# Kernel tuning notes

Measured on AMD Instinct MI355X. Metric: run time of the kernel, lower is better.

Reference implementation:

```python
import jax, jax.numpy as jnp
import numpy as np

N_NODES = 100000
N_EDGES = 1600000
IN_DIM, HID_DIM, OUT_DIM = 128, 64, 64


def setup_inputs() -> dict:
    key = jax.random.key(0)
    ks = jax.random.split(key, 7)
    x = jax.random.normal(ks[0], (N_NODES, IN_DIM), dtype=jnp.float32)
    edge_index = jax.random.randint(ks[1], (2, N_EDGES), 0, N_NODES, dtype=jnp.int64)
    user_idx = jax.random.randint(ks[2], (N_NODES,), 0, N_NODES, dtype=jnp.int64)
    W1 = jax.random.normal(ks[3], (IN_DIM, HID_DIM), dtype=jnp.float32) * (1.0 / np.sqrt(IN_DIM))
    b1 = jax.random.normal(ks[4], (HID_DIM,), dtype=jnp.float32) * 0.02
    W2 = jax.random.normal(ks[5], (HID_DIM, OUT_DIM), dtype=jnp.float32) * (1.0 / np.sqrt(HID_DIM))
    b2 = jax.random.normal(ks[6], (OUT_DIM,), dtype=jnp.float32) * 0.02
    return {"x": x, "edge_index": edge_index, "user_idx": user_idx,
            "W1": W1, "b1": b1, "W2": W2, "b2": b2}


def _gcn_conv(x, edge_index, W, b):
    # PyG GCNConv: linear transform, add self-loops, sym-normalized aggregation.
    N = x.shape[0]
    h = x @ W  # [N, F_out]
    loop = jnp.arange(N, dtype=edge_index.dtype)
    src = jnp.concatenate([edge_index[0], loop])  # [E+N]
    dst = jnp.concatenate([edge_index[1], loop])
    deg = jax.ops.segment_sum(jnp.ones(src.shape[0], dtype=h.dtype), dst, num_segments=N)
    dis = jnp.where(deg > 0, jax.lax.rsqrt(jnp.maximum(deg, 1.0)), 0.0)  # deg^{-1/2}
    norm = dis[src] * dis[dst]  # [E+N]
    msg = h[src] * norm[:, None]  # gather + scale
    out = jax.ops.segment_sum(msg, dst, num_segments=N)  # scatter-add at targets
    return out + b


def _scatter_mean(x, idx, dim_size):
    s = jax.ops.segment_sum(x, idx, num_segments=dim_size)
    cnt = jax.ops.segment_sum(jnp.ones(x.shape[0], dtype=x.dtype), idx, num_segments=dim_size)
    return jnp.where(cnt[:, None] > 0, s / jnp.maximum(cnt[:, None], 1.0), 0.0)


def reference(x, edge_index, user_idx, W1, b1, W2, b2):
    h = _gcn_conv(x, edge_index, W1, b1)
    h = jax.nn.relu(h)
    # dropout is identity in eval mode
    h = _gcn_conv(h, edge_index, W2, b2)
    return _scatter_mean(h, user_idx, h.shape[0])
```

## Files before the change

kernel.cpp:

```cpp
#include <hip/hip_runtime.h>
#include <hip/hip_bf16.h>


#define FEAT 64
#define INDIM 128

#define SCAN_BS 256
#define SCAN_ELEMS 8
#define SCAN_CHUNK (SCAN_BS * SCAN_ELEMS)

#define BIN_SHIFT 9
#define BIN_R 512
#define BIN_TILE 4096
#define BH_TILE 8192

typedef __attribute__((ext_vector_type(8))) short short8;
typedef __attribute__((ext_vector_type(4))) float f32x4;

__device__ __forceinline__ unsigned short f2bf(float f) {
    unsigned u = __float_as_uint(f);
    unsigned r = u + 0x7FFFu + ((u >> 16) & 1u);
    return (unsigned short)(r >> 16);
}
__device__ __forceinline__ float bf2f(unsigned short v) {
    return __uint_as_float(((unsigned)v) << 16);
}


__global__ __launch_bounds__(256) void k_bhist(const int* __restrict__ dst,
                                               int* __restrict__ gbc, int E, int N, int KB) {
    __shared__ int h[256];
    const int tid = threadIdx.x;
    h[tid] = 0;
    __syncthreads();
    const int base = blockIdx.x * BH_TILE;
    #pragma unroll
    for (int t = 0; t < BH_TILE / 256; ++t) {
        int e = base + t * 256 + tid;
        if (e < E) {
            int d = dst[e];
            if ((unsigned)d < (unsigned)N) atomicAdd(&h[d >> BIN_SHIFT], 1);
        }
    }
    __syncthreads();
    if (tid < KB && h[tid]) atomicAdd(&gbc[tid], h[tid]);
}

__global__ __launch_bounds__(256) void k_bscan(const int* __restrict__ gbc,
                                               int* __restrict__ bb,
                                               int* __restrict__ bcur,
                                               int* __restrict__ rpN, int KB) {
    __shared__ int lds[256];
    const int tid = threadIdx.x;
    int v = (tid < KB) ? gbc[tid] : 0;
    lds[tid] = v;
    __syncthreads();
    for (int d = 1; d < 256; d <<= 1) {
        int t = (tid >= d) ? lds[tid - d] : 0;
        __syncthreads();
        lds[tid] += t;
        __syncthreads();
    }
    int excl = lds[tid] - v;
    if (tid < KB) { bb[tid] = excl; bcur[tid] = excl; }
    if (tid == 255) { bb[KB] = lds[255]; *rpN = lds[255]; }
}

__global__ __launch_bounds__(256) void k_binA(const int* __restrict__ src,
                                              const int* __restrict__ dst,
                                              int* __restrict__ bcur,
                                              unsigned* __restrict__ pairs,
                                              int E, int N, int KB) {
    __shared__ unsigned lbuf[BIN_TILE];
    __shared__ unsigned short bkt[BIN_TILE];
    __shared__ int lcnt[256];
    __shared__ int loff[256];
    __shared__ int lbase[256];
    __shared__ int tot;
    const int tid = threadIdx.x;
    const int base = blockIdx.x * BIN_TILE;

    lcnt[tid] = 0;
    __syncthreads();

    int mys[16], myd[16], myb[16];
    #pragma unroll
    for (int t = 0; t < 16; ++t) {
        int e = base + t * 256 + tid;
        int s = 0, d = -1;
        if (e < E) { s = src[e]; d = dst[e]; }
        if ((unsigned)d >= (unsigned)N) d = -1;
        if ((unsigned)s >= (unsigned)N) s = 0;
        mys[t] = s; myd[t] = d;
        myb[t] = (d >= 0) ? (d >> BIN_SHIFT) : -1;
        if (myb[t] >= 0) atomicAdd(&lcnt[myb[t]], 1);
    }
    __syncthreads();

    int v = lcnt[tid];
    loff[tid] = v;
    __syncthreads();
    for (int d = 1; d < 256; d <<= 1) {
        int t2 = (tid >= d) ? loff[tid - d] : 0;
        __syncthreads();
        loff[tid] += t2;
        __syncthreads();
    }
    if (tid == 255) tot = loff[255];
    int excl = loff[tid] - v;
    __syncthreads();
    loff[tid] = excl;
    lcnt[tid] = excl;
    if (tid < KB && v > 0) lbase[tid] = atomicAdd(&bcur[tid], v);
    __syncthreads();

    #pragma unroll
    for (int t = 0; t < 16; ++t) {
        if (myb[t] >= 0) {
            int pos = atomicAdd(&lcnt[myb[t]], 1);
            lbuf[pos] = ((unsigned)mys[t] << BIN_SHIFT) | (unsigned)(myd[t] & (BIN_R - 1));
            bkt[pos] = (unsigned short)myb[t];
        }
    }
    __syncthreads();

    const int T = tot;
    for (int i = tid; i < T; i += 256) {
        int b = bkt[i];
        pairs[lbase[b] + (i - loff[b])] = lbuf[i];
    }
}

__global__ __launch_bounds__(256) void k_binB2(const unsigned* __restrict__ pairs,
                                               const int* __restrict__ bb,
                                               int* __restrict__ rp,
                                               int* __restrict__ col,
                                               float* __restrict__ dis, int N) {
    __shared__ int cnt[BIN_R];
    __shared__ int cur[BIN_R];
    __shared__ int ssum[256];
    const int tid = threadIdx.x;
    const int b = blockIdx.x;
    const int n0 = b << BIN_SHIFT;
    const int n1 = min(n0 + BIN_R, N);
    const int nn = n1 - n0;
    const int e0 = bb[b];
    const int e1 = bb[b + 1];

    for (int i = tid; i < nn; i += 256) cnt[i] = 0;
    __syncthreads();
    for (int i = e0 + tid; i < e1; i += 256) {
        atomicAdd(&cnt[pairs[i] & (BIN_R - 1)], 1);
    }
    __syncthreads();

    const int i0 = 2 * tid;
    int c0 = (i0     < nn) ? cnt[i0]     : 0;
    int c1 = (i0 + 1 < nn) ? cnt[i0 + 1] : 0;
    ssum[tid] = c0 + c1;
    __syncthreads();
    for (int d = 1; d < 256; d <<= 1) {
        int t = (tid >= d) ? ssum[tid - d] : 0;
        __syncthreads();
        ssum[tid] += t;
        __syncthreads();
    }
    int excl = ssum[tid] - (c0 + c1);
    if (i0 < nn) {
        cur[i0] = e0 + excl;
        rp[n0 + i0] = e0 + excl;
        dis[n0 + i0] = rsqrtf((float)c0 + 1.0f);
    }
    if (i0 + 1 < nn) {
        cur[i0 + 1] = e0 + excl + c0;
        rp[n0 + i0 + 1] = e0 + excl + c0;
        dis[n0 + i0 + 1] = rsqrtf((float)c1 + 1.0f);
    }
    __syncthreads();

    for (int i = e0 + tid; i < e1; i += 256) {
        unsigned p = pairs[i];
        int pos = atomicAdd(&cur[p & (BIN_R - 1)], 1);
        col[pos] = (int)(p >> BIN_SHIFT);
    }
}


__global__ __launch_bounds__(256) void k_hist(const int* __restrict__ dst,
                                              int* __restrict__ cntE, int E, int N) {
    int e = blockIdx.x * 256 + threadIdx.x;
    if (e < E) {
        int d = dst[e];
        if ((unsigned)d < (unsigned)N) atomicAdd(&cntE[d], 1);
    }
}
__global__ __launch_bounds__(256) void k_dis(const int* __restrict__ cntE,
                                             float* __restrict__ dis, int N) {
    int i = blockIdx.x * 256 + threadIdx.x;
    if (i < N) dis[i] = rsqrtf((float)cntE[i] + 1.0f);
}
__global__ __launch_bounds__(SCAN_BS) void k_scan1(const int* __restrict__ c,
                                                   int* __restrict__ rp,
                                                   int* __restrict__ ptot, int N) {
    __shared__ int lds[SCAN_BS];
    const int base = blockIdx.x * SCAN_CHUNK;
    const int tb = base + threadIdx.x * SCAN_ELEMS;
    int vals[SCAN_ELEMS];
    int s = 0;
    #pragma unroll
    for (int k = 0; k < SCAN_ELEMS; ++k) {
        int idx = tb + k;
        int v = (idx < N) ? c[idx] : 0;
        vals[k] = s;
        s += v;
    }
    lds[threadIdx.x] = s;
    __syncthreads();
    for (int d = 1; d < SCAN_BS; d <<= 1) {
        int v = (threadIdx.x >= d) ? lds[threadIdx.x - d] : 0;
        __syncthreads();
        lds[threadIdx.x] += v;
        __syncthreads();
    }
    int toff = (threadIdx.x == 0) ? 0 : lds[threadIdx.x - 1];
    #pragma unroll
    for (int k = 0; k < SCAN_ELEMS; ++k) {
        int idx = tb + k;
        if (idx < N) rp[idx] = toff + vals[k];
    }
    if (threadIdx.x == SCAN_BS - 1) ptot[blockIdx.x] = lds[SCAN_BS - 1];
}
__global__ __launch_bounds__(1024) void k_scan2(int* __restrict__ ptot,
                                                int* __restrict__ poff,
                                                int* __restrict__ rpN, int nb) {
    __shared__ int lds[1024];
    int tid = threadIdx.x;
    lds[tid] = (tid < nb) ? ptot[tid] : 0;
    __syncthreads();
    for (int d = 1; d < 1024; d <<= 1) {
        int v = (tid >= d) ? lds[tid - d] : 0;
        __syncthreads();
        lds[tid] += v;
        __syncthreads();
    }
    if (tid < nb) poff[tid] = (tid == 0) ? 0 : lds[tid - 1];
    if (tid == nb - 1) *rpN = lds[tid];
}
__global__ __launch_bounds__(SCAN_BS) void k_scan3(int* __restrict__ rp,
                                                   const int* __restrict__ poff, int N) {
    int off = poff[blockIdx.x];
    const int tb = blockIdx.x * SCAN_CHUNK + threadIdx.x * SCAN_ELEMS;
    #pragma unroll
    for (int k = 0; k < SCAN_ELEMS; ++k) {
        int idx = tb + k;
        if (idx < N) rp[idx] += off;
    }
}
__global__ __launch_bounds__(256) void k_fill(const int* __restrict__ src,
                                              const int* __restrict__ dst,
                                              const int* __restrict__ rp,
                                              int* __restrict__ tmp,
                                              int* __restrict__ col, int E, int N) {
    int e = blockIdx.x * 256 + threadIdx.x;
    if (e >= E) return;
    int s = src[e], d = dst[e];
    if ((unsigned)s >= (unsigned)N) s = 0;
    if ((unsigned)d >= (unsigned)N) return;
    int r = atomicAdd(&tmp[d], 1);
    col[rp[d] + r] = s;
}

__global__ __launch_bounds__(256) void k_ucnt(const int* __restrict__ uidx,
                                              float* __restrict__ cntf, int N) {
    int i = blockIdx.x * 256 + threadIdx.x;
    if (i < N) {
        int u = uidx[i];
        if ((unsigned)u < (unsigned)N) atomicAdd(&cntf[u], 1.0f);
    }
}


__global__ __launch_bounds__(256) void k_gemm1(const float* __restrict__ x,
                                               const float* __restrict__ W,
                                               const float* __restrict__ scale,
                                               unsigned short* __restrict__ out, int N) {
    __shared__ short wf[4 * 4 * 64 * 8];
    const int tid = threadIdx.x;
    for (int i = tid; i < INDIM * FEAT; i += 256) {
        int k = i >> 6, n = i & 63;
        int ct = n >> 4, kc = k >> 5, r = k & 31;
        int owner = ((r >> 3) << 4) | (n & 15);
        wf[(((ct << 2) | kc) * 64 + owner) * 8 + (r & 7)] = (short)f2bf(W[i]);
    }
    __syncthreads();

    const int lane = tid & 63;
    const int m = lane & 15, q = lane >> 4;
    const int row0 = blockIdx.x * 64 + (tid >> 6) * 16;

    short8 bfr[4][4];
    #pragma unroll
    for (int ct = 0; ct < 4; ++ct)
        #pragma unroll
        for (int kc = 0; kc < 4; ++kc)
            bfr[ct][kc] = *reinterpret_cast<const short8*>(&wf[(((ct << 2) | kc) * 64 + lane) * 8]);

    int gr = row0 + m;
    int rl = gr < N ? gr : (N - 1);
    const float* xp = x + (long)rl * INDIM + q * 8;

    f32x4 acc[4] = {{0,0,0,0},{0,0,0,0},{0,0,0,0},{0,0,0,0}};
    #pragma unroll
    for (int kc = 0; kc < 4; ++kc) {
        float4 v0 = *reinterpret_cast<const float4*>(xp + kc * 32);
        float4 v1 = *reinterpret_cast<const float4*>(xp + kc * 32 + 4);
        short8 a;
        a[0]=(short)f2bf(v0.x); a[1]=(short)f2bf(v0.y); a[2]=(short)f2bf(v0.z); a[3]=(short)f2bf(v0.w);
        a[4]=(short)f2bf(v1.x); a[5]=(short)f2bf(v1.y); a[6]=(short)f2bf(v1.z); a[7]=(short)f2bf(v1.w);
        #pragma unroll
        for (int ct = 0; ct < 4; ++ct)
            acc[ct] = __builtin_amdgcn_mfma_f32_16x16x32_bf16(a, bfr[ct][kc], acc[ct], 0, 0, 0);
    }

    #pragma unroll
    for (int reg = 0; reg < 4; ++reg) {
        int row = row0 + q * 4 + reg;
        if (row < N) {
            float sc = scale[row];
            #pragma unroll
            for (int ct = 0; ct < 4; ++ct)
                out[(long)row * FEAT + ct * 16 + m] = f2bf(acc[ct][reg] * sc);
        }
    }
}

__global__ __launch_bounds__(256) void k_gemm2(const float* __restrict__ h,
                                               const float* __restrict__ W,
                                               const float* __restrict__ scale,
                                               unsigned short* __restrict__ out, int N) {
    __shared__ short wf[4 * 2 * 64 * 8];
    const int tid = threadIdx.x;
    for (int i = tid; i < FEAT * FEAT; i += 256) {
        int k = i >> 6, n = i & 63;
        int ct = n >> 4, kc = k >> 5, r = k & 31;
        int owner = ((r >> 3) << 4) | (n & 15);
        wf[(((ct << 1) | kc) * 64 + owner) * 8 + (r & 7)] = (short)f2bf(W[i]);
    }
    __syncthreads();

    const int lane = tid & 63;
    const int m = lane & 15, q = lane >> 4;
    const int row0 = blockIdx.x * 64 + (tid >> 6) * 16;

    short8 bfr[4][2];
    #pragma unroll
    for (int ct = 0; ct < 4; ++ct)
        #pragma unroll
        for (int kc = 0; kc < 2; ++kc)
            bfr[ct][kc] = *reinterpret_cast<const short8*>(&wf[(((ct << 1) | kc) * 64 + lane) * 8]);

    int gr = row0 + m;
    int rl = gr < N ? gr : (N - 1);
    const float* hp = h + (long)rl * FEAT + q * 8;

    f32x4 acc[4] = {{0,0,0,0},{0,0,0,0},{0,0,0,0},{0,0,0,0}};
    #pragma unroll
    for (int kc = 0; kc < 2; ++kc) {
        float4 v0 = *reinterpret_cast<const float4*>(hp + kc * 32);
        float4 v1 = *reinterpret_cast<const float4*>(hp + kc * 32 + 4);
        short8 a;
        a[0]=(short)f2bf(v0.x); a[1]=(short)f2bf(v0.y); a[2]=(short)f2bf(v0.z); a[3]=(short)f2bf(v0.w);
        a[4]=(short)f2bf(v1.x); a[5]=(short)f2bf(v1.y); a[6]=(short)f2bf(v1.z); a[7]=(short)f2bf(v1.w);
        #pragma unroll
        for (int ct = 0; ct < 4; ++ct)
            acc[ct] = __builtin_amdgcn_mfma_f32_16x16x32_bf16(a, bfr[ct][kc], acc[ct], 0, 0, 0);
    }

    #pragma unroll
    for (int reg = 0; reg < 4; ++reg) {
        int row = row0 + q * 4 + reg;
        if (row < N) {
            float sc = scale[row];
            #pragma unroll
            for (int ct = 0; ct < 4; ++ct)
                out[(long)row * FEAT + ct * 16 + m] = f2bf(acc[ct][reg] * sc);
        }
    }
}


#define AGG_BODY(SELF_INIT)                                                      \
    const int lane = threadIdx.x & 63;                                           \
    const int q2 = lane >> 3;                                                    \
    const int ol = lane & 7;                                                     \
    const int jb = rp[i], je = rp[i + 1];                                        \
    float a0=0.f,a1=0.f,a2=0.f,a3=0.f,a4=0.f,a5=0.f,a6=0.f,a7=0.f;               \
    if (q2 == 0) { SELF_INIT }                                                   \
    for (int j0 = jb; j0 < je; j0 += 16) {                                       \
        int ja = j0 + q2, jb2 = j0 + 8 + q2;                                     \
        int ca = (ja  < je) ? col[ja]  : i;  float ma = (ja  < je) ? 1.f : 0.f;  \
        int cb = (jb2 < je) ? col[jb2] : i;  float mb = (jb2 < je) ? 1.f : 0.f;  \
        uint4 ra = *reinterpret_cast<const uint4*>(A + (long)ca * FEAT + 8 * ol);\
        uint4 rb = *reinterpret_cast<const uint4*>(A + (long)cb * FEAT + 8 * ol);\
        a0 = fmaf(ma, bf2f((unsigned short)ra.x),         a0);                   \
        a1 = fmaf(ma, bf2f((unsigned short)(ra.x >> 16)), a1);                   \
        a2 = fmaf(ma, bf2f((unsigned short)ra.y),         a2);                   \
        a3 = fmaf(ma, bf2f((unsigned short)(ra.y >> 16)), a3);                   \
        a4 = fmaf(ma, bf2f((unsigned short)ra.z),         a4);                   \
        a5 = fmaf(ma, bf2f((unsigned short)(ra.z >> 16)), a5);                   \
        a6 = fmaf(ma, bf2f((unsigned short)ra.w),         a6);                   \
        a7 = fmaf(ma, bf2f((unsigned short)(ra.w >> 16)), a7);                   \
        a0 = fmaf(mb, bf2f((unsigned short)rb.x),         a0);                   \
        a1 = fmaf(mb, bf2f((unsigned short)(rb.x >> 16)), a1);                   \
        a2 = fmaf(mb, bf2f((unsigned short)rb.y),         a2);                   \
        a3 = fmaf(mb, bf2f((unsigned short)(rb.y >> 16)), a3);                   \
        a4 = fmaf(mb, bf2f((unsigned short)rb.z),         a4);                   \
        a5 = fmaf(mb, bf2f((unsigned short)(rb.z >> 16)), a5);                   \
        a6 = fmaf(mb, bf2f((unsigned short)rb.w),         a6);                   \
        a7 = fmaf(mb, bf2f((unsigned short)(rb.w >> 16)), a7);                   \
    }                                                                            \
    a0 += __shfl_xor(a0, 8);  a1 += __shfl_xor(a1, 8);                           \
    a2 += __shfl_xor(a2, 8);  a3 += __shfl_xor(a3, 8);                           \
    a4 += __shfl_xor(a4, 8);  a5 += __shfl_xor(a5, 8);                           \
    a6 += __shfl_xor(a6, 8);  a7 += __shfl_xor(a7, 8);                           \
    a0 += __shfl_xor(a0, 16); a1 += __shfl_xor(a1, 16);                          \
    a2 += __shfl_xor(a2, 16); a3 += __shfl_xor(a3, 16);                          \
    a4 += __shfl_xor(a4, 16); a5 += __shfl_xor(a5, 16);                          \
    a6 += __shfl_xor(a6, 16); a7 += __shfl_xor(a7, 16);                          \
    a0 += __shfl_xor(a0, 32); a1 += __shfl_xor(a1, 32);                          \
    a2 += __shfl_xor(a2, 32); a3 += __shfl_xor(a3, 32);                          \
    a4 += __shfl_xor(a4, 32); a5 += __shfl_xor(a5, 32);                          \
    a6 += __shfl_xor(a6, 32); a7 += __shfl_xor(a7, 32);

__global__ __launch_bounds__(256) void k_agg1(const unsigned short* __restrict__ A,
                                              const int* __restrict__ rp,
                                              const int* __restrict__ col,
                                              const float* __restrict__ dis,
                                              const float* __restrict__ bias,
                                              float* __restrict__ H, int N) {
    int i = blockIdx.x * 4 + (threadIdx.x >> 6);
    if (i >= N) return;
    AGG_BODY(
        uint4 rv = *reinterpret_cast<const uint4*>(A + (long)i * FEAT + 8 * ol);
        a0 = bf2f((unsigned short)rv.x); a1 = bf2f((unsigned short)(rv.x >> 16));
        a2 = bf2f((unsigned short)rv.y); a3 = bf2f((unsigned short)(rv.y >> 16));
        a4 = bf2f((unsigned short)rv.z); a5 = bf2f((unsigned short)(rv.z >> 16));
        a6 = bf2f((unsigned short)rv.w); a7 = bf2f((unsigned short)(rv.w >> 16));
    )
    if (q2 == 0) {
        float di = dis[i];
        float4 b4a = *reinterpret_cast<const float4*>(bias + 8 * ol);
        float4 b4b = *reinterpret_cast<const float4*>(bias + 8 * ol + 4);
        float4 o0, o1;
        o0.x = fmaxf(fmaf(di, a0, b4a.x), 0.f);
        o0.y = fmaxf(fmaf(di, a1, b4a.y), 0.f);
        o0.z = fmaxf(fmaf(di, a2, b4a.z), 0.f);
        o0.w = fmaxf(fmaf(di, a3, b4a.w), 0.f);
        o1.x = fmaxf(fmaf(di, a4, b4b.x), 0.f);
        o1.y = fmaxf(fmaf(di, a5, b4b.y), 0.f);
        o1.z = fmaxf(fmaf(di, a6, b4b.z), 0.f);
        o1.w = fmaxf(fmaf(di, a7, b4b.w), 0.f);
        *reinterpret_cast<float4*>(H + (long)i * FEAT + 8 * ol)     = o0;
        *reinterpret_cast<float4*>(H + (long)i * FEAT + 8 * ol + 4) = o1;
    }
}

__global__ __launch_bounds__(256) void k_agg2s(const unsigned short* __restrict__ A,
                                               const int* __restrict__ rp,
                                               const int* __restrict__ col,
                                               const float* __restrict__ dis,
                                               const float* __restrict__ bias,
                                               const int* __restrict__ uidx,
                                               float* __restrict__ S, int N) {
    int i = blockIdx.x * 4 + (threadIdx.x >> 6);
    if (i >= N) return;
    AGG_BODY(
        uint4 rv = *reinterpret_cast<const uint4*>(A + (long)i * FEAT + 8 * ol);
        a0 = bf2f((unsigned short)rv.x); a1 = bf2f((unsigned short)(rv.x >> 16));
        a2 = bf2f((unsigned short)rv.y); a3 = bf2f((unsigned short)(rv.y >> 16));
        a4 = bf2f((unsigned short)rv.z); a5 = bf2f((unsigned short)(rv.z >> 16));
        a6 = bf2f((unsigned short)rv.w); a7 = bf2f((unsigned short)(rv.w >> 16));
    )
    int u = uidx[i];
    if ((unsigned)u < (unsigned)N) {
        float di = dis[i];
        float v = (q2 == 0) ? a0 : (q2 == 1) ? a1 : (q2 == 2) ? a2 : (q2 == 3) ? a3
                : (q2 == 4) ? a4 : (q2 == 5) ? a5 : (q2 == 6) ? a6 : a7;
        int f = 8 * ol + q2;
        atomicAdd(&S[(long)u * FEAT + f], fmaf(di, v, bias[f]));
    }
}

__global__ __launch_bounds__(256) void k_final(float* __restrict__ S,
                                               const float* __restrict__ cnt, int N) {
    long idx = (long)blockIdx.x * 256 + threadIdx.x;
    if (idx >= (long)N * FEAT) return;
    int i = (int)(idx >> 6);
    float c = cnt[i];
    S[idx] = (c > 0.f) ? S[idx] / c : 0.f;
}

extern "C" void kernel_launch(void* const* d_in, const int* in_sizes, int n_in,
                              void* d_out, int out_size, void* d_ws, size_t ws_size,
                              hipStream_t stream) {
    const float* x   = (const float*)d_in[0];
    const int* edge  = (const int*)d_in[1];
    const int* uidx  = (const int*)d_in[2];
    const float* W1  = (const float*)d_in[3];
    const float* b1  = (const float*)d_in[4];
    const float* W2  = (const float*)d_in[5];
    const float* b2  = (const float*)d_in[6];
    float* out       = (float*)d_out;

    const int N = in_sizes[2];
    const int E = in_sizes[1] / 2;
    const int* src = edge;
    const int* dst = edge + E;

    const size_t fbuf = (size_t)N * FEAT * sizeof(float);
    const size_t abuf = (size_t)N * FEAT * sizeof(unsigned short);
    const long NF = (long)N * FEAT;
    const int gNF = (int)((NF + 255) / 256);
    const int gE  = (E + 255) / 256;
    const int gN  = (N + 255) / 256;
    const int gN4 = (N + 3) / 4;
    const int gG  = (N + 63) / 64;
    const int nbScan = (N + SCAN_CHUNK - 1) / SCAN_CHUNK;
    const int KB = (N + BIN_R - 1) >> BIN_SHIFT;

    auto align256 = [](size_t v) { return (v + 255) & ~(size_t)255; };

    char* w = (char*)d_ws;
    size_t o = 0;
    float* dis  = (float*)(w + o); o = align256(o + (size_t)N * 4);
    float* cntf = (float*)(w + o); o = align256(o + (size_t)N * 4);
    int*   rp   = (int*)  (w + o); o = align256(o + (size_t)(N + 1) * 4);
    int*   cntE = (int*)  (w + o); o = align256(o + (size_t)N * 4);
    int*   ptot = (int*)  (w + o); o = align256(o + (size_t)1024 * 4);
    int*   poff = (int*)  (w + o); o = align256(o + (size_t)1024 * 4);
    int*   col  = (int*)  (w + o); o = align256(o + (size_t)E * 4);
    size_t apsz = (size_t)E * 4 > abuf ? (size_t)E * 4 : abuf;
    char*  Ap   = w + o;           o = align256(o + apsz);
    const size_t need = o;
    int* gbc  = cntE;
    int* bb   = ptot;
    int* bcur = poff;
    unsigned* pairs = (unsigned*)Ap;
    unsigned short* A = (unsigned short*)Ap;

    if (ws_size >= need && KB <= 256 && N <= (1 << (32 - BIN_SHIFT - 1))) {
        hipMemsetAsync(gbc, 0, (size_t)KB * 4, stream);
        k_bhist<<<(E + BH_TILE - 1) / BH_TILE, 256, 0, stream>>>(dst, gbc, E, N, KB);
        k_bscan<<<1, 256, 0, stream>>>(gbc, bb, bcur, rp + N, KB);
        k_binA <<<(E + BIN_TILE - 1) / BIN_TILE, 256, 0, stream>>>(src, dst, bcur, pairs, E, N, KB);
        k_binB2<<<KB, 256, 0, stream>>>(pairs, bb, rp, col, dis, N);
        hipMemsetAsync(cntf, 0, (size_t)N * 4, stream);
        k_ucnt <<<gN, 256, 0, stream>>>(uidx, cntf, N);

        k_gemm1<<<gG, 256, 0, stream>>>(x, W1, dis, A, N);
        k_agg1 <<<gN4, 256, 0, stream>>>(A, rp, col, dis, b1, out, N);

        k_gemm2<<<gG, 256, 0, stream>>>(out, W2, dis, A, N);
        hipMemsetAsync(out, 0, fbuf, stream);
        k_agg2s<<<gN4, 256, 0, stream>>>(A, rp, col, dis, b2, uidx, out, N);
        k_final<<<gNF, 256, 0, stream>>>(out, cntf, N);
    } else {
        hipMemsetAsync(cntE, 0, (size_t)N * 4, stream);
        k_hist <<<gE, 256, 0, stream>>>(dst, cntE, E, N);
        k_dis  <<<gN, 256, 0, stream>>>(cntE, dis, N);
        k_scan1<<<nbScan, SCAN_BS, 0, stream>>>(cntE, rp, ptot, N);
        k_scan2<<<1, 1024, 0, stream>>>(ptot, poff, rp + N, nbScan);
        k_scan3<<<nbScan, SCAN_BS, 0, stream>>>(rp, poff, N);
        hipMemsetAsync(cntE, 0, (size_t)N * 4, stream);
        k_fill <<<gE, 256, 0, stream>>>(src, dst, rp, cntE, col, E, N);
        hipMemsetAsync(cntf, 0, (size_t)N * 4, stream);
        k_ucnt <<<gN, 256, 0, stream>>>(uidx, cntf, N);
        k_gemm1<<<gG, 256, 0, stream>>>(x, W1, dis, A, N);
        k_agg1 <<<gN4, 256, 0, stream>>>(A, rp, col, dis, b1, out, N);
        k_gemm2<<<gG, 256, 0, stream>>>(out, W2, dis, A, N);
        hipMemsetAsync(out, 0, fbuf, stream);
        k_agg2s<<<gN4, 256, 0, stream>>>(A, rp, col, dis, b2, uidx, out, N);
        k_final<<<gNF, 256, 0, stream>>>(out, cntf, N);
    }
}
```

Before: 307.1 us.

## Store layer-1 output as bf16, fold mean division into scatter, retune binning

```diff
diff --git a/kernel.cpp b/kernel.cpp
--- a/kernel.cpp
+++ b/kernel.cpp
@@ -11,8 +11,8 @@
 
 #define BIN_SHIFT 9
 #define BIN_R 512
-#define BIN_TILE 4096
-#define BH_TILE 8192
+#define BIN_TILE 2048
+#define BH_TILE 2048
 
 typedef __attribute__((ext_vector_type(8))) short short8;
 typedef __attribute__((ext_vector_type(4))) float f32x4;
@@ -83,9 +83,9 @@
     lcnt[tid] = 0;
     __syncthreads();
 
-    int mys[16], myd[16], myb[16];
-    #pragma unroll
-    for (int t = 0; t < 16; ++t) {
+    int mys[BIN_TILE / 256], myd[BIN_TILE / 256], myb[BIN_TILE / 256];
+    #pragma unroll
+    for (int t = 0; t < BIN_TILE / 256; ++t) {
         int e = base + t * 256 + tid;
         int s = 0, d = -1;
         if (e < E) { s = src[e]; d = dst[e]; }
@@ -115,7 +115,7 @@
     __syncthreads();
 
     #pragma unroll
-    for (int t = 0; t < 16; ++t) {
+    for (int t = 0; t < BIN_TILE / 256; ++t) {
         if (myb[t] >= 0) {
             int pos = atomicAdd(&lcnt[myb[t]], 1);
             lbuf[pos] = ((unsigned)mys[t] << BIN_SHIFT) | (unsigned)(myd[t] & (BIN_R - 1));
@@ -131,11 +131,11 @@
     }
 }
 
-__global__ __launch_bounds__(256) void k_binB2(const unsigned* __restrict__ pairs,
-                                               const int* __restrict__ bb,
-                                               int* __restrict__ rp,
-                                               int* __restrict__ col,
-                                               float* __restrict__ dis, int N) {
+__global__ __launch_bounds__(1024) void k_binB2(const unsigned* __restrict__ pairs,
+                                                const int* __restrict__ bb,
+                                                int* __restrict__ rp,
+                                                int* __restrict__ col,
+                                                float* __restrict__ dis, int N) {
     __shared__ int cnt[BIN_R];
     __shared__ int cur[BIN_R];
     __shared__ int ssum[256];
@@ -147,38 +147,44 @@
     const int e0 = bb[b];
     const int e1 = bb[b + 1];
 
-    for (int i = tid; i < nn; i += 256) cnt[i] = 0;
-    __syncthreads();
-    for (int i = e0 + tid; i < e1; i += 256) {
+    for (int i = tid; i < nn; i += 1024) cnt[i] = 0;
+    __syncthreads();
+    for (int i = e0 + tid; i < e1; i += 1024) {
         atomicAdd(&cnt[pairs[i] & (BIN_R - 1)], 1);
     }
     __syncthreads();
 
     const int i0 = 2 * tid;
-    int c0 = (i0     < nn) ? cnt[i0]     : 0;
-    int c1 = (i0 + 1 < nn) ? cnt[i0 + 1] : 0;
-    ssum[tid] = c0 + c1;
+    int c0 = 0, c1 = 0;
+    if (tid < 256) {
+        c0 = (i0     < nn) ? cnt[i0]     : 0;
+        c1 = (i0 + 1 < nn) ? cnt[i0 + 1] : 0;
+        ssum[tid] = c0 + c1;
+    }
     __syncthreads();
     for (int d = 1; d < 256; d <<= 1) {
-        int t = (tid >= d) ? ssum[tid - d] : 0;
-        __syncthreads();
-        ssum[tid] += t;
-        __syncthreads();
-    }
-    int excl = ssum[tid] - (c0 + c1);
-    if (i0 < nn) {
-        cur[i0] = e0 + excl;
-        rp[n0 + i0] = e0 + excl;
-        dis[n0 + i0] = rsqrtf((float)c0 + 1.0f);
-    }
-    if (i0 + 1 < nn) {
-        cur[i0 + 1] = e0 + excl + c0;
-        rp[n0 + i0 + 1] = e0 + excl + c0;
-        dis[n0 + i0 + 1] = rsqrtf((float)c1 + 1.0f);
-    }
-    __syncthreads();
-
-    for (int i = e0 + tid; i < e1; i += 256) {
+        int t = 0;
+        if (tid < 256 && tid >= d) t = ssum[tid - d];
+        __syncthreads();
+        if (tid < 256) ssum[tid] += t;
+        __syncthreads();
+    }
+    if (tid < 256) {
+        int excl = ssum[tid] - (c0 + c1);
+        if (i0 < nn) {
+            cur[i0] = e0 + excl;
+            rp[n0 + i0] = e0 + excl;
+            dis[n0 + i0] = rsqrtf((float)c0 + 1.0f);
+        }
+        if (i0 + 1 < nn) {
+            cur[i0 + 1] = e0 + excl + c0;
+            rp[n0 + i0 + 1] = e0 + excl + c0;
+            dis[n0 + i0 + 1] = rsqrtf((float)c1 + 1.0f);
+        }
+    }
+    __syncthreads();
+
+    for (int i = e0 + tid; i < e1; i += 1024) {
         unsigned p = pairs[i];
         int pos = atomicAdd(&cur[p & (BIN_R - 1)], 1);
         col[pos] = (int)(p >> BIN_SHIFT);
@@ -279,6 +285,14 @@
     }
 }
 
+__global__ __launch_bounds__(256) void k_inv(float* __restrict__ c, int N) {
+    int i = blockIdx.x * 256 + threadIdx.x;
+    if (i < N) {
+        float v = c[i];
+        c[i] = (v > 0.f) ? (1.0f / v) : 0.f;
+    }
+}
+
 
 __global__ __launch_bounds__(256) void k_gemm1(const float* __restrict__ x,
                                                const float* __restrict__ W,
@@ -334,7 +348,7 @@
     }
 }
 
-__global__ __launch_bounds__(256) void k_gemm2(const float* __restrict__ h,
+__global__ __launch_bounds__(256) void k_gemm2(const unsigned short* __restrict__ h,
                                                const float* __restrict__ W,
                                                const float* __restrict__ scale,
                                                unsigned short* __restrict__ out, int N) {
@@ -361,16 +375,12 @@
 
     int gr = row0 + m;
     int rl = gr < N ? gr : (N - 1);
-    const float* hp = h + (long)rl * FEAT + q * 8;
+    const unsigned short* hp = h + (long)rl * FEAT + q * 8;
 
     f32x4 acc[4] = {{0,0,0,0},{0,0,0,0},{0,0,0,0},{0,0,0,0}};
     #pragma unroll
     for (int kc = 0; kc < 2; ++kc) {
-        float4 v0 = *reinterpret_cast<const float4*>(hp + kc * 32);
-        float4 v1 = *reinterpret_cast<const float4*>(hp + kc * 32 + 4);
-        short8 a;
-        a[0]=(short)f2bf(v0.x); a[1]=(short)f2bf(v0.y); a[2]=(short)f2bf(v0.z); a[3]=(short)f2bf(v0.w);
-        a[4]=(short)f2bf(v1.x); a[5]=(short)f2bf(v1.y); a[6]=(short)f2bf(v1.z); a[7]=(short)f2bf(v1.w);
+        short8 a = *reinterpret_cast<const short8*>(hp + kc * 32);
         #pragma unroll
         for (int ct = 0; ct < 4; ++ct)
             acc[ct] = __builtin_amdgcn_mfma_f32_16x16x32_bf16(a, bfr[ct][kc], acc[ct], 0, 0, 0);
@@ -389,6 +399,16 @@
 }
 
 
+#define ACC8(r, mm)                                                              \
+    a0 = fmaf(mm, bf2f((unsigned short)(r).x),         a0);                      \
+    a1 = fmaf(mm, bf2f((unsigned short)((r).x >> 16)), a1);                      \
+    a2 = fmaf(mm, bf2f((unsigned short)(r).y),         a2);                      \
+    a3 = fmaf(mm, bf2f((unsigned short)((r).y >> 16)), a3);                      \
+    a4 = fmaf(mm, bf2f((unsigned short)(r).z),         a4);                      \
+    a5 = fmaf(mm, bf2f((unsigned short)((r).z >> 16)), a5);                      \
+    a6 = fmaf(mm, bf2f((unsigned short)(r).w),         a6);                      \
+    a7 = fmaf(mm, bf2f((unsigned short)((r).w >> 16)), a7);
+
 #define AGG_BODY(SELF_INIT)                                                      \
     const int lane = threadIdx.x & 63;                                           \
     const int q2 = lane >> 3;                                                    \
@@ -396,28 +416,20 @@
     const int jb = rp[i], je = rp[i + 1];                                        \
     float a0=0.f,a1=0.f,a2=0.f,a3=0.f,a4=0.f,a5=0.f,a6=0.f,a7=0.f;               \
     if (q2 == 0) { SELF_INIT }                                                   \
-    for (int j0 = jb; j0 < je; j0 += 16) {                                       \
-        int ja = j0 + q2, jb2 = j0 + 8 + q2;                                     \
-        int ca = (ja  < je) ? col[ja]  : i;  float ma = (ja  < je) ? 1.f : 0.f;  \
-        int cb = (jb2 < je) ? col[jb2] : i;  float mb = (jb2 < je) ? 1.f : 0.f;  \
-        uint4 ra = *reinterpret_cast<const uint4*>(A + (long)ca * FEAT + 8 * ol);\
-        uint4 rb = *reinterpret_cast<const uint4*>(A + (long)cb * FEAT + 8 * ol);\
-        a0 = fmaf(ma, bf2f((unsigned short)ra.x),         a0);                   \
-        a1 = fmaf(ma, bf2f((unsigned short)(ra.x >> 16)), a1);                   \
-        a2 = fmaf(ma, bf2f((unsigned short)ra.y),         a2);                   \
-        a3 = fmaf(ma, bf2f((unsigned short)(ra.y >> 16)), a3);                   \
-        a4 = fmaf(ma, bf2f((unsigned short)ra.z),         a4);                   \
-        a5 = fmaf(ma, bf2f((unsigned short)(ra.z >> 16)), a5);                   \
-        a6 = fmaf(ma, bf2f((unsigned short)ra.w),         a6);                   \
-        a7 = fmaf(ma, bf2f((unsigned short)(ra.w >> 16)), a7);                   \
-        a0 = fmaf(mb, bf2f((unsigned short)rb.x),         a0);                   \
-        a1 = fmaf(mb, bf2f((unsigned short)(rb.x >> 16)), a1);                   \
-        a2 = fmaf(mb, bf2f((unsigned short)rb.y),         a2);                   \
-        a3 = fmaf(mb, bf2f((unsigned short)(rb.y >> 16)), a3);                   \
-        a4 = fmaf(mb, bf2f((unsigned short)rb.z),         a4);                   \
-        a5 = fmaf(mb, bf2f((unsigned short)(rb.z >> 16)), a5);                   \
-        a6 = fmaf(mb, bf2f((unsigned short)rb.w),         a6);                   \
-        a7 = fmaf(mb, bf2f((unsigned short)(rb.w >> 16)), a7);                   \
+    for (int j0 = jb; j0 < je; j0 += 32) {                                       \
+        int j1 = j0 + q2, j2 = j0 + 8 + q2, j3 = j0 + 16 + q2, j4 = j0 + 24 + q2;\
+        int c1 = (j1 < je) ? col[j1] : i;  float m1 = (j1 < je) ? 1.f : 0.f;     \
+        int c2 = (j2 < je) ? col[j2] : i;  float m2 = (j2 < je) ? 1.f : 0.f;     \
+        int c3 = (j3 < je) ? col[j3] : i;  float m3 = (j3 < je) ? 1.f : 0.f;     \
+        int c4 = (j4 < je) ? col[j4] : i;  float m4 = (j4 < je) ? 1.f : 0.f;     \
+        uint4 r1 = *reinterpret_cast<const uint4*>(A + (long)c1 * FEAT + 8 * ol);\
+        uint4 r2 = *reinterpret_cast<const uint4*>(A + (long)c2 * FEAT + 8 * ol);\
+        uint4 r3 = *reinterpret_cast<const uint4*>(A + (long)c3 * FEAT + 8 * ol);\
+        uint4 r4 = *reinterpret_cast<const uint4*>(A + (long)c4 * FEAT + 8 * ol);\
+        ACC8(r1, m1)                                                             \
+        ACC8(r2, m2)                                                             \
+        ACC8(r3, m3)                                                             \
+        ACC8(r4, m4)                                                             \
     }                                                                            \
     a0 += __shfl_xor(a0, 8);  a1 += __shfl_xor(a1, 8);                           \
     a2 += __shfl_xor(a2, 8);  a3 += __shfl_xor(a3, 8);                           \
@@ -437,7 +449,7 @@
                                               const int* __restrict__ col,
                                               const float* __restrict__ dis,
                                               const float* __restrict__ bias,
-                                              float* __restrict__ H, int N) {
+                                              unsigned short* __restrict__ H, int N) {
     int i = blockIdx.x * 4 + (threadIdx.x >> 6);
     if (i >= N) return;
     AGG_BODY(
@@ -451,17 +463,16 @@
         float di = dis[i];
         float4 b4a = *reinterpret_cast<const float4*>(bias + 8 * ol);
         float4 b4b = *reinterpret_cast<const float4*>(bias + 8 * ol + 4);
-        float4 o0, o1;
-        o0.x = fmaxf(fmaf(di, a0, b4a.x), 0.f);
-        o0.y = fmaxf(fmaf(di, a1, b4a.y), 0.f);
-        o0.z = fmaxf(fmaf(di, a2, b4a.z), 0.f);
-        o0.w = fmaxf(fmaf(di, a3, b4a.w), 0.f);
-        o1.x = fmaxf(fmaf(di, a4, b4b.x), 0.f);
-        o1.y = fmaxf(fmaf(di, a5, b4b.y), 0.f);
-        o1.z = fmaxf(fmaf(di, a6, b4b.z), 0.f);
-        o1.w = fmaxf(fmaf(di, a7, b4b.w), 0.f);
-        *reinterpret_cast<float4*>(H + (long)i * FEAT + 8 * ol)     = o0;
-        *reinterpret_cast<float4*>(H + (long)i * FEAT + 8 * ol + 4) = o1;
+        uint4 o;
+        o.x = (unsigned)f2bf(fmaxf(fmaf(di, a0, b4a.x), 0.f))
+            | ((unsigned)f2bf(fmaxf(fmaf(di, a1, b4a.y), 0.f)) << 16);
+        o.y = (unsigned)f2bf(fmaxf(fmaf(di, a2, b4a.z), 0.f))
+            | ((unsigned)f2bf(fmaxf(fmaf(di, a3, b4a.w), 0.f)) << 16);
+        o.z = (unsigned)f2bf(fmaxf(fmaf(di, a4, b4b.x), 0.f))
+            | ((unsigned)f2bf(fmaxf(fmaf(di, a5, b4b.y), 0.f)) << 16);
+        o.w = (unsigned)f2bf(fmaxf(fmaf(di, a6, b4b.z), 0.f))
+            | ((unsigned)f2bf(fmaxf(fmaf(di, a7, b4b.w), 0.f)) << 16);
+        *reinterpret_cast<uint4*>(H + (long)i * FEAT + 8 * ol) = o;
     }
 }
 
@@ -471,6 +482,7 @@
                                                const float* __restrict__ dis,
                                                const float* __restrict__ bias,
                                                const int* __restrict__ uidx,
+                                               const float* __restrict__ invc,
                                                float* __restrict__ S, int N) {
     int i = blockIdx.x * 4 + (threadIdx.x >> 6);
     if (i >= N) return;
@@ -484,20 +496,12 @@
     int u = uidx[i];
     if ((unsigned)u < (unsigned)N) {
         float di = dis[i];
+        float w = invc[u];
         float v = (q2 == 0) ? a0 : (q2 == 1) ? a1 : (q2 == 2) ? a2 : (q2 == 3) ? a3
                 : (q2 == 4) ? a4 : (q2 == 5) ? a5 : (q2 == 6) ? a6 : a7;
         int f = 8 * ol + q2;
-        atomicAdd(&S[(long)u * FEAT + f], fmaf(di, v, bias[f]));
-    }
-}
-
-__global__ __launch_bounds__(256) void k_final(float* __restrict__ S,
-                                               const float* __restrict__ cnt, int N) {
-    long idx = (long)blockIdx.x * 256 + threadIdx.x;
-    if (idx >= (long)N * FEAT) return;
-    int i = (int)(idx >> 6);
-    float c = cnt[i];
-    S[idx] = (c > 0.f) ? S[idx] / c : 0.f;
+        atomicAdd(&S[(long)u * FEAT + f], w * fmaf(di, v, bias[f]));
+    }
 }
 
 extern "C" void kernel_launch(void* const* d_in, const int* in_sizes, int n_in,
@@ -519,8 +523,6 @@
 
     const size_t fbuf = (size_t)N * FEAT * sizeof(float);
     const size_t abuf = (size_t)N * FEAT * sizeof(unsigned short);
-    const long NF = (long)N * FEAT;
-    const int gNF = (int)((NF + 255) / 256);
     const int gE  = (E + 255) / 256;
     const int gN  = (N + 255) / 256;
     const int gN4 = (N + 3) / 4;
@@ -547,23 +549,24 @@
     int* bcur = poff;
     unsigned* pairs = (unsigned*)Ap;
     unsigned short* A = (unsigned short*)Ap;
+    unsigned short* Hb = (unsigned short*)out;
 
     if (ws_size >= need && KB <= 256 && N <= (1 << (32 - BIN_SHIFT - 1))) {
         hipMemsetAsync(gbc, 0, (size_t)KB * 4, stream);
         k_bhist<<<(E + BH_TILE - 1) / BH_TILE, 256, 0, stream>>>(dst, gbc, E, N, KB);
         k_bscan<<<1, 256, 0, stream>>>(gbc, bb, bcur, rp + N, KB);
         k_binA <<<(E + BIN_TILE - 1) / BIN_TILE, 256, 0, stream>>>(src, dst, bcur, pairs, E, N, KB);
-        k_binB2<<<KB, 256, 0, stream>>>(pairs, bb, rp, col, dis, N);
+        k_binB2<<<KB, 1024, 0, stream>>>(pairs, bb, rp, col, dis, N);
         hipMemsetAsync(cntf, 0, (size_t)N * 4, stream);
         k_ucnt <<<gN, 256, 0, stream>>>(uidx, cntf, N);
+        k_inv  <<<gN, 256, 0, stream>>>(cntf, N);
 
         k_gemm1<<<gG, 256, 0, stream>>>(x, W1, dis, A, N);
-        k_agg1 <<<gN4, 256, 0, stream>>>(A, rp, col, dis, b1, out, N);
-
-        k_gemm2<<<gG, 256, 0, stream>>>(out, W2, dis, A, N);
+        k_agg1 <<<gN4, 256, 0, stream>>>(A, rp, col, dis, b1, Hb, N);
+
+        k_gemm2<<<gG, 256, 0, stream>>>(Hb, W2, dis, A, N);
         hipMemsetAsync(out, 0, fbuf, stream);
-        k_agg2s<<<gN4, 256, 0, stream>>>(A, rp, col, dis, b2, uidx, out, N);
-        k_final<<<gNF, 256, 0, stream>>>(out, cntf, N);
+        k_agg2s<<<gN4, 256, 0, stream>>>(A, rp, col, dis, b2, uidx, cntf, out, N);
     } else {
         hipMemsetAsync(cntE, 0, (size_t)N * 4, stream);
         k_hist <<<gE, 256, 0, stream>>>(dst, cntE, E, N);
@@ -575,11 +578,11 @@
         k_fill <<<gE, 256, 0, stream>>>(src, dst, rp, cntE, col, E, N);
         hipMemsetAsync(cntf, 0, (size_t)N * 4, stream);
         k_ucnt <<<gN, 256, 0, stream>>>(uidx, cntf, N);
+        k_inv  <<<gN, 256, 0, stream>>>(cntf, N);
         k_gemm1<<<gG, 256, 0, stream>>>(x, W1, dis, A, N);
-        k_agg1 <<<gN4, 256, 0, stream>>>(A, rp, col, dis, b1, out, N);
-        k_gemm2<<<gG, 256, 0, stream>>>(out, W2, dis, A, N);
+        k_agg1 <<<gN4, 256, 0, stream>>>(A, rp, col, dis, b1, Hb, N);
+        k_gemm2<<<gG, 256, 0, stream>>>(Hb, W2, dis, A, N);
         hipMemsetAsync(out, 0, fbuf, stream);
-        k_agg2s<<<gN4, 256, 0, stream>>>(A, rp, col, dis, b2, uidx, out, N);
-        k_final<<<gNF, 256, 0, stream>>>(out, cntf, N);
-    }
-}
+        k_agg2s<<<gN4, 256, 0, stream>>>(A, rp, col, dis, b2, uidx, cntf, out, N);
+    }
+}
```

New measurement: 286.7 us. 6.6% less time.
